# Kernel optimization log

Hardware: AMD Instinct MI355X
Metric: run time of the kernel (lower is better)

## Reference

```python
import jax, jax.numpy as jnp
from jax import lax
import numpy as np

EPS_START, EPS_END, EPS_DECAY = 1.0, 0.05, 10000.0


def gru_step(x, h, w_ih, w_hh, b_ih, b_hh):
    # PyTorch GRUCell math; gates stacked as [r, z, n]
    gi = x @ w_ih.T + b_ih
    gh = h @ w_hh.T + b_hh
    i_r, i_z, i_n = jnp.split(gi, 3, axis=1)
    h_r, h_z, h_n = jnp.split(gh, 3, axis=1)
    r = jax.nn.sigmoid(i_r + h_r)
    z = jax.nn.sigmoid(i_z + h_z)
    n = jnp.tanh(i_n + r * h_n)
    return (1.0 - z) * n + z * h


def setup_inputs() -> dict:
    key = jax.random.key(0)
    ks = jax.random.split(key, 7)
    V, E, H = 32000, 256, 512
    s = 0.05
    return {
        "embedding": jax.random.normal(ks[0], (V, E), jnp.float32) * s,
        "w_ih": jax.random.normal(ks[1], (3 * H, E), jnp.float32) * s,
        "w_hh": jax.random.normal(ks[2], (3 * H, H), jnp.float32) * s,
        "b_ih": jax.random.normal(ks[3], (3 * H,), jnp.float32) * s,
        "b_hh": jax.random.normal(ks[4], (3 * H,), jnp.float32) * s,
        "w_out": jax.random.normal(ks[5], (V, H), jnp.float32) * s,
        "b_out": jax.random.normal(ks[6], (V,), jnp.float32) * s,
        "seq_len": 256,
        "batch_size": 512,
    }


def reference(embedding, w_ih, w_hh, b_ih, b_hh, w_out, b_out, seq_len, batch_size):
    V, E = embedding.shape
    H = w_hh.shape[1]
    B = batch_size
    log_unif = jnp.float32(np.log(V))  # -log(vocab_size) fill for epsilon-greedy

    keys = jax.random.split(jax.random.key(42), seq_len)
    ts = jnp.arange(seq_len, dtype=jnp.float32)

    h0 = jnp.zeros((B, H), jnp.float32)
    x0 = jnp.broadcast_to(embedding[0], (B, E))  # start token id 0

    def step(carry, inp):
        h, x = carry
        t, k = inp
        k_eps, k_gum = jax.random.split(k)
        h = gru_step(x, h, w_ih, w_hh, b_ih, b_hh)
        logp = jax.nn.log_softmax(h @ w_out.T + b_out, axis=1)  # [B, V]
        eps_t = EPS_END + (EPS_START - EPS_END) * jnp.exp(-4.0 * t / EPS_DECAY)
        draw = eps_t >= jax.random.uniform(k_eps, (B,))
        masked = jnp.where(draw[:, None], -log_unif, logp)
        g = jax.random.gumbel(k_gum, (B, V), jnp.float32)
        sampled = jnp.argmax(masked + g, axis=1)  # [B] int
        lp = jnp.take_along_axis(logp, sampled[:, None], axis=1)[:, 0]
        x_next = embedding[sampled]
        return (h, x_next), (sampled, lp)

    _, (samples, lps) = lax.scan(step, (h0, x0), (ts, keys))
    return samples.T, lps.T  # [B, S] each
```

## Files before the change

kernel.cpp:

```cpp
#include <hip/hip_runtime.h>
#include <math.h>
#include <stdio.h>

#ifndef JAX_PARTITIONABLE
#define JAX_PARTITIONABLE 1
#endif

namespace {

constexpr int B  = 512;
constexpr int S  = 256;
constexpr int E  = 256;
constexpr int H  = 512;
constexpr int V  = 32000;
constexpr int G3 = 3 * H;
constexpr int VBLK = 64;
constexpr int BBLK = 256;
constexpr int NCH  = V / VBLK;
constexpr int NDMAX = 96;

typedef __bf16 bf16x8 __attribute__((ext_vector_type(8)));
typedef float  f32x4  __attribute__((ext_vector_type(4)));
typedef unsigned u32x4 __attribute__((ext_vector_type(4)));

__device__ __forceinline__ void tf2x32(unsigned k0, unsigned k1,
                                       unsigned x0, unsigned x1,
                                       unsigned& o0, unsigned& o1) {
  unsigned ks2 = k0 ^ k1 ^ 0x1BD11BDAu;
  x0 += k0; x1 += k1;
#define TFR(r) { x0 += x1; x1 = (x1 << (r)) | (x1 >> (32 - (r))); x1 ^= x0; }
  TFR(13) TFR(15) TFR(26) TFR(6)   x0 += k1;  x1 += ks2 + 1u;
  TFR(17) TFR(29) TFR(16) TFR(24)  x0 += ks2; x1 += k0 + 2u;
  TFR(13) TFR(15) TFR(26) TFR(6)   x0 += k0;  x1 += k1 + 3u;
  TFR(17) TFR(29) TFR(16) TFR(24)  x0 += k1;  x1 += ks2 + 4u;
  TFR(13) TFR(15) TFR(26) TFR(6)   x0 += ks2; x1 += k0 + 5u;
#undef TFR
  o0 = x0; o1 = x1;
}

__device__ __forceinline__ unsigned rbits(unsigned g0, unsigned g1,
                                          unsigned b, unsigned v) {
#if JAX_PARTITIONABLE
  unsigned y0, y1;
  tf2x32(g0, g1, 0u, b * (unsigned)V + v, y0, y1);
  return y0 ^ y1;
#else
  const unsigned N2 = (unsigned)(B/2) * (unsigned)V;
  unsigned ii = b * (unsigned)V + v;
  unsigned jj = (b < 256) ? ii : ii - N2;
  unsigned y0, y1;
  tf2x32(g0, g1, jj, N2 + jj, y0, y1);
  return (b < 256) ? y0 : y1;
#endif
}

__device__ __forceinline__ float u01_from_bits(unsigned bits) {
  return __uint_as_float(0x3f800000u | (bits >> 9)) - 1.0f;
}

__device__ __forceinline__ float gumbel_exact(unsigned bits) {
  float u = u01_from_bits(bits);
  if (u == 0.0f) u = 1.1754943508222875e-38f;
  float w = (float)(-log((double)u));
  return (float)(-log((double)w));
}

__device__ __forceinline__ float gumbel_fast(unsigned bits) {
  float u = u01_from_bits(bits);
  if (u == 0.0f) u = 1.1754943508222875e-38f;
  float w = -__logf(u);
  return -__logf(w);
}

__device__ __forceinline__ unsigned short f2bf(float f) {
  unsigned u = __float_as_uint(f);
  unsigned r = (u + 0x7fffu + ((u >> 16) & 1u)) >> 16;
  return (unsigned short)r;
}

__device__ __forceinline__ void glds16(const unsigned short* g,
                                       unsigned short* l) {
  __builtin_amdgcn_global_load_lds(
      (const __attribute__((address_space(1))) unsigned int*)g,
      (__attribute__((address_space(3))) unsigned int*)l, 16, 0, 0);
}

__device__ __forceinline__ size_t frag_off(int row, int k, int kTiles) {
  return ((size_t)((row >> 4) * kTiles + (k >> 5)) * 64
          + (row & 15) + 16 * ((k >> 3) & 3)) * 8 + (k & 7);
}

__global__ void k_init_rng(unsigned* __restrict__ kq, unsigned* __restrict__ ke) {
  int t = threadIdx.x;
  unsigned h0, h1, e0, e1, g0, g1;
#if JAX_PARTITIONABLE
  tf2x32(0u, 42u, 0u, (unsigned)t, h0, h1);
  tf2x32(h0, h1, 0u, 0u, e0, e1);
  tf2x32(h0, h1, 0u, 1u, g0, g1);
#else
  unsigned a0, a1, b0, b1;
  if (t < 128) {
    tf2x32(0u, 42u, (unsigned)(2*t),   (unsigned)(256+2*t), a0, a1);
    tf2x32(0u, 42u, (unsigned)(2*t+1), (unsigned)(257+2*t), b0, b1);
    h0 = a0; h1 = b0;
  } else {
    int j = 2*t - 256;
    tf2x32(0u, 42u, (unsigned)j,     (unsigned)(256+j), a0, a1);
    tf2x32(0u, 42u, (unsigned)(j+1), (unsigned)(257+j), b0, b1);
    h0 = a1; h1 = b1;
  }
  unsigned p0, p1, q0, q1;
  tf2x32(h0, h1, 0u, 2u, p0, p1);
  tf2x32(h0, h1, 1u, 3u, q0, q1);
  e0 = p0; e1 = q0; g0 = p1; g1 = q1;
#endif
  ke[2*t] = e0; ke[2*t+1] = e1;
  kq[2*t] = g0; kq[2*t+1] = g1;
}

__global__ void k_init_draws(const unsigned* __restrict__ ke,
                             unsigned char* __restrict__ draws) {
  int t = blockIdx.x;
  int b = threadIdx.x;
  unsigned k0 = ke[2*t], k1 = ke[2*t+1];
  unsigned bits, y0, y1;
#if JAX_PARTITIONABLE
  tf2x32(k0, k1, 0u, (unsigned)b, y0, y1);
  bits = y0 ^ y1;
#else
  if (b < 256) { tf2x32(k0, k1, (unsigned)b,       (unsigned)(256+b), y0, y1); bits = y0; }
  else         { tf2x32(k0, k1, (unsigned)(b-256), (unsigned)b,       y0, y1); bits = y1; }
#endif
  float u   = u01_from_bits(bits);
  float tf  = (float)t;
  float ex  = expf(__fmul_rn(-4.0f, tf) / 10000.0f);
  float eps = __fadd_rn(0.05f, __fmul_rn(0.95f, ex));
  draws[t*B + b] = (eps >= u) ? 1 : 0;
}

__global__ void k_init_nd(const unsigned char* __restrict__ draws,
                          int* __restrict__ nd_slot) {
  int t = blockIdx.x;
  if (threadIdx.x != 0) return;
  int cnt = 0;
  for (int b = 0; b < B; b++) {
    if (!draws[t*B + b] && cnt < NDMAX) nd_slot[t*B + b] = cnt++;
    else nd_slot[t*B + b] = -1;
  }
}

__global__ __launch_bounds__(256) void k_pre_argmax(
    const unsigned* __restrict__ kq, const unsigned char* __restrict__ draws,
    int* __restrict__ pre) {
  const int job  = blockIdx.x * 4 + (threadIdx.x >> 6);
  const int lane = threadIdx.x & 63;
  const int t = job >> 9, b = job & (B - 1);
  if (!draws[t*B + b]) { if (lane == 0) pre[job] = -1; return; }
  const unsigned g0 = kq[2*t], g1 = kq[2*t+1];
  unsigned best = 0u; int bv = V;
  for (int v = lane; v < V; v += 64) {
    unsigned bits = rbits(g0, g1, (unsigned)b, (unsigned)v) >> 9;
    if (bits > best || (bits == best && v < bv)) { best = bits; bv = v; }
  }
#pragma unroll
  for (int m = 1; m < 64; m <<= 1) {
    unsigned ob = __shfl_xor(best, m, 64);
    int      ov = __shfl_xor(bv,   m, 64);
    if (ob > best || (ob == best && ov < bv)) { best = ob; bv = ov; }
  }
  if (lane == 0) pre[job] = bv;
}

__global__ void k_init_state(const float* __restrict__ emb,
                             float* __restrict__ x, float* __restrict__ h) {
  int b = blockIdx.x, tid = threadIdx.x;
  x[b*E + tid] = emb[tid];
  h[b*H + tid] = 0.0f;
  h[b*H + 256 + tid] = 0.0f;
}

__global__ void k_cast_w(const float* __restrict__ w,
                         unsigned short* __restrict__ w_sw) {
  int g = blockIdx.x*256 + threadIdx.x;
  int v  = g >> 6;
  int k0 = (g & 63) * 8;
  const float* src = w + (size_t)v*H + k0;
  union { unsigned short s[8]; u32x4 vv; } u;
#pragma unroll
  for (int e = 0; e < 8; e++) u.s[e] = f2bf(src[e]);
  *(u32x4*)&w_sw[frag_off(v, k0, H/32)] = u.vv;
}

__global__ __launch_bounds__(256) void k_gates(
    const float* __restrict__ x, const float* __restrict__ h,
    const float* __restrict__ w_ih, const float* __restrict__ w_hh,
    const float* __restrict__ b_ih, const float* __restrict__ b_hh,
    float* __restrict__ gi, float* __restrict__ gh) {
  const int z = blockIdx.z;
  const float* A    = z ? h    : x;
  const float* W    = z ? w_hh : w_ih;
  const float* bias = z ? b_hh : b_ih;
  float*       C    = z ? gh   : gi;
  const int K       = z ? H    : E;

  __shared__ __align__(16) float As[16][68];
  __shared__ __align__(16) float Ws[16][68];
  const int tid = threadIdx.x;
  const int tx = tid & 15, ty = tid >> 4;
  const int row0 = blockIdx.y * 64, col0 = blockIdx.x * 64;
  float acc[4][4] = {};
  for (int k0 = 0; k0 < K; k0 += 16) {
#pragma unroll
    for (int l = 0; l < 4; l++) {
      int idx = tid + l*256;
      int r = idx >> 4, kk = idx & 15;
      As[kk][r] = A[(row0 + r)*K + k0 + kk];
      Ws[kk][r] = W[(col0 + r)*K + k0 + kk];
    }
    __syncthreads();
#pragma unroll
    for (int kk = 0; kk < 16; kk++) {
      const float4 av = *(const float4*)&As[kk][ty*4];
      const float4 wv = *(const float4*)&Ws[kk][tx*4];
      const float a[4] = {av.x, av.y, av.z, av.w};
      const float w[4] = {wv.x, wv.y, wv.z, wv.w};
#pragma unroll
      for (int i = 0; i < 4; i++)
#pragma unroll
        for (int j = 0; j < 4; j++) acc[i][j] = fmaf(a[i], w[j], acc[i][j]);
    }
    __syncthreads();
  }
#pragma unroll
  for (int i = 0; i < 4; i++) {
    int r = row0 + ty*4 + i;
#pragma unroll
    for (int j = 0; j < 4; j++) {
      int c = col0 + tx*4 + j;
      C[r*G3 + c] = __fadd_rn(acc[i][j], bias[c]);
    }
  }
}

__device__ __forceinline__ float sigm_acc(float v) {
  return (float)(1.0 / (1.0 + exp(-(double)v)));
}
__device__ __forceinline__ float tanh_acc(float v) {
  return (float)tanh((double)v);
}

__global__ void k_gru_update(const float* __restrict__ gi,
                             const float* __restrict__ gh,
                             float* __restrict__ h,
                             unsigned short* __restrict__ h_sw) {
  int g = blockIdx.x*256 + threadIdx.x;
  int b  = g >> 6;
  int j0 = (g & 63) * 8;
  const float* gib = gi + (size_t)b*G3;
  const float* ghb = gh + (size_t)b*G3;
  float hn[8];
  union { unsigned short s[8]; u32x4 vv; } u;
#pragma unroll
  for (int e = 0; e < 8; e++) {
    int j = j0 + e;
    float r  = sigm_acc(__fadd_rn(gib[j],     ghb[j]));
    float zz = sigm_acc(__fadd_rn(gib[H+j],   ghb[H+j]));
    float nn = tanh_acc(__fadd_rn(gib[2*H+j], __fmul_rn(r, ghb[2*H+j])));
    float hv = h[(size_t)b*H + j];
    float t1 = __fmul_rn(__fsub_rn(1.0f, zz), nn);
    float t2 = __fmul_rn(zz, hv);
    hn[e] = __fadd_rn(t1, t2);
    u.s[e] = f2bf(hn[e]);
  }
#pragma unroll
  for (int e = 0; e < 8; e++) h[(size_t)b*H + j0 + e] = hn[e];
  *(u32x4*)&h_sw[frag_off(b, j0, H/32)] = u.vv;
}

__global__ __launch_bounds__(256) void k_mfma_logits(
    const unsigned short* __restrict__ h_sw,
    const unsigned short* __restrict__ w_sw,
    const float* __restrict__ b_out,
    const unsigned* __restrict__ kq,
    const int* __restrict__ pre_t,
    const int* __restrict__ nd_slot_t,
    float* __restrict__ pmax, float* __restrict__ psum,
    float* __restrict__ plog,
    float* __restrict__ nd_keys, float* __restrict__ nd_kmax, int t) {
  const int vblk = blockIdx.x;
  const int bblk = blockIdx.y;
  const int tid  = threadIdx.x;
  const int lane = tid & 63, w = tid >> 6;
  const int quad = lane >> 4, l15 = lane & 15;

  __shared__ __align__(16) unsigned short wt[2][4*512];

  f32x4 acc[4][4] = {};

  const int mtBase = bblk*16 + w*4;
  const int ntBase = vblk*4;
  const unsigned short* hp = h_sw + (size_t)mtBase*16*512 + lane*8;
  const unsigned short* wstage = w_sw + (size_t)(ntBase + w)*16*512 + lane*8;
  unsigned short* ldst = &wt[0][0] + tid*8;

  glds16(wstage, ldst);
  bf16x8 afc[4];
#pragma unroll
  for (int mt = 0; mt < 4; mt++)
    afc[mt] = __builtin_bit_cast(bf16x8, *(const u32x4*)(hp + (size_t)(mt*16)*512));

#pragma unroll 1
  for (int kt = 0; kt < 15; kt++) {
    const int p = kt & 1;
    __syncthreads();
    glds16(wstage + (size_t)(kt + 1)*512, ldst + (p ^ 1)*2048);
    bf16x8 afn[4];
#pragma unroll
    for (int mt = 0; mt < 4; mt++)
      afn[mt] = __builtin_bit_cast(bf16x8,
          *(const u32x4*)(hp + (size_t)(mt*16 + kt + 1)*512));
    bf16x8 bfv[4];
#pragma unroll
    for (int nt = 0; nt < 4; nt++)
      bfv[nt] = __builtin_bit_cast(bf16x8,
          *(const u32x4*)&wt[p][nt*512 + lane*8]);
#pragma unroll
    for (int mt = 0; mt < 4; mt++)
#pragma unroll
      for (int nt = 0; nt < 4; nt++)
        acc[mt][nt] = __builtin_amdgcn_mfma_f32_16x16x32_bf16(
            afc[mt], bfv[nt], acc[mt][nt], 0, 0, 0);
#pragma unroll
    for (int mt = 0; mt < 4; mt++) afc[mt] = afn[mt];
  }
  {
    __syncthreads();
    bf16x8 bfv[4];
#pragma unroll
    for (int nt = 0; nt < 4; nt++)
      bfv[nt] = __builtin_bit_cast(bf16x8,
          *(const u32x4*)&wt[1][nt*512 + lane*8]);
#pragma unroll
    for (int mt = 0; mt < 4; mt++)
#pragma unroll
      for (int nt = 0; nt < 4; nt++)
        acc[mt][nt] = __builtin_amdgcn_mfma_f32_16x16x32_bf16(
            afc[mt], bfv[nt], acc[mt][nt], 0, 0, 0);
  }

  const int bW = bblk*256 + w*64;
  const int vW = vblk*64;
  const unsigned g0 = kq[2*t], g1 = kq[2*t+1];
  float bias[4];
#pragma unroll
  for (int nt = 0; nt < 4; nt++) bias[nt] = b_out[vW + nt*16 + l15];

#pragma unroll
  for (int mt = 0; mt < 4; mt++) {
#pragma unroll
    for (int r = 0; r < 4; r++) {
      const int b = bW + mt*16 + quad*4 + r;
      float lg[4];
#pragma unroll
      for (int nt = 0; nt < 4; nt++) lg[nt] = acc[mt][nt][r] + bias[nt];
      float lmax = fmaxf(fmaxf(lg[0], lg[1]), fmaxf(lg[2], lg[3]));
#pragma unroll
      for (int m = 1; m < 16; m <<= 1) lmax = fmaxf(lmax, __shfl_xor(lmax, m, 64));
      float ls = 0.0f;
#pragma unroll
      for (int nt = 0; nt < 4; nt++) ls += __expf(lg[nt] - lmax);
#pragma unroll
      for (int m = 1; m < 16; m <<= 1) ls += __shfl_xor(ls, m, 64);
      if (l15 == 0) { pmax[b*NCH + vblk] = lmax; psum[b*NCH + vblk] = ls; }
      const int pr = pre_t[b];
      if (pr >= 0) {
        int rel = pr - vW;
        if (rel >= 0 && rel < 64 && (rel & 15) == l15) plog[b] = lg[rel >> 4];
      } else {
        const int slot = nd_slot_t[b];
        if (slot >= 0) {
          float key[4];
#pragma unroll
          for (int nt = 0; nt < 4; nt++)
            key[nt] = lg[nt] + gumbel_fast(
                rbits(g0, g1, (unsigned)b, (unsigned)(vW + nt*16 + l15)));
          float* dst = nd_keys + (size_t)slot*V + vW + l15;
#pragma unroll
          for (int nt = 0; nt < 4; nt++) dst[nt*16] = key[nt];
          float kmx = fmaxf(fmaxf(key[0], key[1]), fmaxf(key[2], key[3]));
#pragma unroll
          for (int m = 1; m < 16; m <<= 1) kmx = fmaxf(kmx, __shfl_xor(kmx, m, 64));
          if (l15 == 0) nd_kmax[slot*NCH + vblk] = kmx;
        }
      }
    }
  }
}

__global__ __launch_bounds__(256) void k_finish(
    const float* __restrict__ pmax, const float* __restrict__ psum,
    const float* __restrict__ plog,
    const int* __restrict__ pre_t, const int* __restrict__ nd_slot_t,
    const float* __restrict__ nd_keys, const float* __restrict__ nd_kmax,
    const unsigned* __restrict__ kq,
    const float* __restrict__ h, const float* __restrict__ w_out,
    const float* __restrict__ b_out,
    const float* __restrict__ emb, float* __restrict__ x,
    float* __restrict__ out_samples, float* __restrict__ out_lps, int t) {
  const int b = blockIdx.x;
  const int tid = threadIdx.x;
  __shared__ float sA[256];
  __shared__ int   cand[160];
  __shared__ float cand_key[160], cand_lg[160];
  __shared__ int   ccnt;
  __shared__ int   s_samp;
  __shared__ float s_blog;

  float m = -INFINITY;
  for (int c = tid; c < NCH; c += 256) m = fmaxf(m, pmax[b*NCH + c]);
  sA[tid] = m; __syncthreads();
  for (int s = 128; s > 0; s >>= 1) {
    if (tid < s) sA[tid] = fmaxf(sA[tid], sA[tid+s]);
    __syncthreads();
  }
  const float M = sA[0];
  __syncthreads();
  float sum = 0.0f;
  for (int c = tid; c < NCH; c += 256)
    sum += psum[b*NCH + c] * expf(pmax[b*NCH + c] - M);
  sA[tid] = sum; __syncthreads();
  for (int s = 128; s > 0; s >>= 1) {
    if (tid < s) sA[tid] += sA[tid+s];
    __syncthreads();
  }
  const float SUM = sA[0];
  __syncthreads();

  const int pr = pre_t[b];
  if (pr >= 0) {
    if (tid == 0) { s_samp = pr; s_blog = plog[b]; }
  } else {
    const int slot = nd_slot_t[b];
    if (slot < 0) {
      if (tid == 0) { s_samp = 0; s_blog = plog[b]; }
    } else {
      const unsigned g0 = kq[2*t], g1 = kq[2*t+1];
      if (tid == 0) ccnt = 0;
      float km = -INFINITY;
      for (int c = tid; c < NCH; c += 256) km = fmaxf(km, nd_kmax[slot*NCH + c]);
      sA[tid] = km; __syncthreads();
      for (int s = 128; s > 0; s >>= 1) {
        if (tid < s) sA[tid] = fmaxf(sA[tid], sA[tid+s]);
        __syncthreads();
      }
      const float thr = sA[0] - 0.0859375f;
      __syncthreads();
      const float* keys = nd_keys + (size_t)slot*V;
      for (int c = tid; c < NCH; c += 256) {
        if (nd_kmax[slot*NCH + c] >= thr) {
          for (int j = 0; j < VBLK; j++) {
            float k = keys[c*VBLK + j];
            if (k >= thr) {
              int p = atomicAdd(&ccnt, 1);
              if (p < 160) cand[p] = c*VBLK + j;
            }
          }
        }
      }
      __syncthreads();
      const int nc = min(ccnt, 160);
      const int wid = tid >> 6, lane = tid & 63;
      for (int c = wid; c < nc; c += 4) {
        const int v = cand[c];
        const float* wr = w_out + (size_t)v*H;
        const float* hr = h + (size_t)b*H;
        float s = 0.0f;
#pragma unroll
        for (int i = 0; i < 8; i++) s = fmaf(hr[lane + 64*i], wr[lane + 64*i], s);
#pragma unroll
        for (int mm = 1; mm < 64; mm <<= 1) s += __shfl_xor(s, mm, 64);
        if (lane == 0) {
          float logit = __fadd_rn(s, b_out[v]);
          float key   = __fadd_rn(logit,
                          gumbel_exact(rbits(g0, g1, (unsigned)b, (unsigned)v)));
          cand_key[c] = key; cand_lg[c] = logit;
        }
      }
      __syncthreads();
      if (tid == 0) {
        float bk = -INFINITY; int bv = V; float bl = 0.0f;
        for (int c = 0; c < nc; c++) {
          float k = cand_key[c]; int v = cand[c];
          if (k > bk || (k == bk && v < bv)) { bk = k; bv = v; bl = cand_lg[c]; }
        }
        s_samp = bv; s_blog = bl;
      }
    }
  }
  __syncthreads();
  const int sampled = s_samp;
  if (tid == 0) {
    float lse = (float)log((double)SUM);
    float lp  = __fsub_rn(__fsub_rn(s_blog, M), lse);
    out_samples[b*S + t] = (float)sampled;
    out_lps[b*S + t]     = lp;
  }
  x[b*E + tid] = emb[sampled*E + tid];
}

}

extern "C" void kernel_launch(void* const* d_in, const int* in_sizes, int n_in,
                              void* d_out, int out_size, void* d_ws, size_t ws_size,
                              hipStream_t stream) {
  (void)in_sizes; (void)n_in; (void)out_size;
  const float* emb   = (const float*)d_in[0];
  const float* w_ih  = (const float*)d_in[1];
  const float* w_hh  = (const float*)d_in[2];
  const float* b_ih  = (const float*)d_in[3];
  const float* b_hh  = (const float*)d_in[4];
  const float* w_out = (const float*)d_in[5];
  const float* b_out = (const float*)d_in[6];
  float* out = (float*)d_out;

  char* wsb = (char*)d_ws;
  size_t off = 0;
  auto alloc = [&](size_t nbytes) {
    char* p = wsb + off;
    off += (nbytes + 255) & ~size_t(255);
    return p;
  };
  float* h     = (float*)alloc((size_t)B*H*4);
  float* x     = (float*)alloc((size_t)B*E*4);
  float* gi    = (float*)alloc((size_t)B*G3*4);
  float* gh    = (float*)alloc((size_t)B*G3*4);
  unsigned short* h_sw = (unsigned short*)alloc((size_t)B*H*2);
  unsigned short* w_sw = (unsigned short*)alloc((size_t)V*H*2);
  float* pmax  = (float*)alloc((size_t)B*NCH*4);
  float* psum  = (float*)alloc((size_t)B*NCH*4);
  float* plog  = (float*)alloc((size_t)B*4);
  unsigned* kq = (unsigned*)alloc((size_t)S*2*4);
  unsigned* ke = (unsigned*)alloc((size_t)S*2*4);
  unsigned char* draws = (unsigned char*)alloc((size_t)S*B);
  int* pre     = (int*)alloc((size_t)S*B*4);
  int* nd_slot = (int*)alloc((size_t)S*B*4);
  float* nd_keys = (float*)alloc((size_t)NDMAX*V*4);
  float* nd_kmax = (float*)alloc((size_t)NDMAX*NCH*4);
  if (off > ws_size) {
    fprintf(stderr, "kernel_launch: workspace too small (need %zu, have %zu)\n",
            off, ws_size);
    return;
  }

  k_init_rng<<<1, S, 0, stream>>>(kq, ke);
  k_init_draws<<<S, B, 0, stream>>>(ke, draws);
  k_init_nd<<<S, 64, 0, stream>>>(draws, nd_slot);
  k_pre_argmax<<<(S*B)/4, 256, 0, stream>>>(kq, draws, pre);
  k_init_state<<<B, 256, 0, stream>>>(emb, x, h);
  k_cast_w<<<(V*H/8)/256, 256, 0, stream>>>(w_out, w_sw);

  for (int t = 0; t < S; t++) {
    k_gates<<<dim3(G3/64, B/64, 2), 256, 0, stream>>>(x, h, w_ih, w_hh,
                                                      b_ih, b_hh, gi, gh);
    k_gru_update<<<(B*H/8)/256, 256, 0, stream>>>(gi, gh, h, h_sw);
    k_mfma_logits<<<dim3(V/VBLK, B/BBLK), 256, 0, stream>>>(
        h_sw, w_sw, b_out, kq, pre + t*B, nd_slot + t*B,
        pmax, psum, plog, nd_keys, nd_kmax, t);
    k_finish<<<B, 256, 0, stream>>>(pmax, psum, plog, pre + t*B, nd_slot + t*B,
                                    nd_keys, nd_kmax, kq, h, w_out, b_out,
                                    emb, x, out, out + (size_t)B*S, t);
  }
}
```

Baseline: 36.20 ms.

## Fuse next-step epsilon argmax into logits kernel, swizzle blocks, retile gates GEMM

The upfront k_pre_argmax over all timesteps is replaced. It now handles only step 0, and each later step's uniform-draw argmax runs in extra blocks of k_mfma_logits for timestep t+1, so that work overlaps the logits GEMM. The logits grid is remapped with an XCD-style swizzle of the linear block id into (vblk, bblk). k_gates moves to 512 threads computing 2x4 outputs each, with float4 stores. The risks are imbalance between the RNG blocks and the MFMA blocks, plus extra launched blocks that exit immediately.

```diff
diff --git a/kernel.cpp b/kernel.cpp
--- a/kernel.cpp
+++ b/kernel.cpp
@@ -191,7 +191,7 @@
   *(u32x4*)&w_sw[frag_off(v, k0, H/32)] = u.vv;
 }
 
-__global__ __launch_bounds__(256) void k_gates(
+__global__ __launch_bounds__(512) void k_gates(
     const float* __restrict__ x, const float* __restrict__ h,
     const float* __restrict__ w_ih, const float* __restrict__ w_hh,
     const float* __restrict__ b_ih, const float* __restrict__ b_hh,
@@ -208,11 +208,11 @@
   const int tid = threadIdx.x;
   const int tx = tid & 15, ty = tid >> 4;
   const int row0 = blockIdx.y * 64, col0 = blockIdx.x * 64;
-  float acc[4][4] = {};
+  float acc[2][4] = {};
   for (int k0 = 0; k0 < K; k0 += 16) {
 #pragma unroll
-    for (int l = 0; l < 4; l++) {
-      int idx = tid + l*256;
+    for (int l = 0; l < 2; l++) {
+      int idx = tid + l*512;
       int r = idx >> 4, kk = idx & 15;
       As[kk][r] = A[(row0 + r)*K + k0 + kk];
       Ws[kk][r] = W[(col0 + r)*K + k0 + kk];
@@ -220,25 +220,27 @@
     __syncthreads();
 #pragma unroll
     for (int kk = 0; kk < 16; kk++) {
-      const float4 av = *(const float4*)&As[kk][ty*4];
+      const float2 av = *(const float2*)&As[kk][ty*2];
       const float4 wv = *(const float4*)&Ws[kk][tx*4];
-      const float a[4] = {av.x, av.y, av.z, av.w};
+      const float a[2] = {av.x, av.y};
       const float w[4] = {wv.x, wv.y, wv.z, wv.w};
 #pragma unroll
-      for (int i = 0; i < 4; i++)
+      for (int i = 0; i < 2; i++)
 #pragma unroll
         for (int j = 0; j < 4; j++) acc[i][j] = fmaf(a[i], w[j], acc[i][j]);
     }
     __syncthreads();
   }
 #pragma unroll
-  for (int i = 0; i < 4; i++) {
-    int r = row0 + ty*4 + i;
-#pragma unroll
-    for (int j = 0; j < 4; j++) {
-      int c = col0 + tx*4 + j;
-      C[r*G3 + c] = __fadd_rn(acc[i][j], bias[c]);
-    }
+  for (int i = 0; i < 2; i++) {
+    int r = row0 + ty*2 + i;
+    int c = col0 + tx*4;
+    float4 o;
+    o.x = __fadd_rn(acc[i][0], bias[c + 0]);
+    o.y = __fadd_rn(acc[i][1], bias[c + 1]);
+    o.z = __fadd_rn(acc[i][2], bias[c + 2]);
+    o.w = __fadd_rn(acc[i][3], bias[c + 3]);
+    *(float4*)&C[r*G3 + c] = o;
   }
 }
 
@@ -282,18 +284,55 @@
     const unsigned short* __restrict__ w_sw,
     const float* __restrict__ b_out,
     const unsigned* __restrict__ kq,
-    const int* __restrict__ pre_t,
+    const unsigned char* __restrict__ draws,
+    int* __restrict__ pre,
     const int* __restrict__ nd_slot_t,
     float* __restrict__ pmax, float* __restrict__ psum,
     float* __restrict__ plog,
     float* __restrict__ nd_keys, float* __restrict__ nd_kmax, int t) {
-  const int vblk = blockIdx.x;
-  const int bblk = blockIdx.y;
+  __shared__ __align__(16) unsigned short wt[2][4*512];
   const int tid  = threadIdx.x;
+
+  if (blockIdx.y == 0) {
+    const int tn = t + 1;
+    if (tn >= S) return;
+    const int b = blockIdx.x;
+    if (!draws[tn*B + b]) { if (tid == 0) pre[tn*B + b] = -1; return; }
+    const unsigned g0 = kq[2*tn], g1 = kq[2*tn+1];
+    unsigned best = 0u; int bv = V;
+    for (int v = tid; v < V; v += 256) {
+      unsigned bits = rbits(g0, g1, (unsigned)b, (unsigned)v) >> 9;
+      if (bits > best || (bits == best && v < bv)) { best = bits; bv = v; }
+    }
+#pragma unroll
+    for (int m = 1; m < 64; m <<= 1) {
+      unsigned ob = __shfl_xor(best, m, 64);
+      int      ov = __shfl_xor(bv,   m, 64);
+      if (ob > best || (ob == best && ov < bv)) { best = ob; bv = ov; }
+    }
+    unsigned* sb = (unsigned*)&wt[0][0];
+    int*      sv = (int*)&wt[1][0];
+    const int wv2 = tid >> 6;
+    if ((tid & 63) == 0) { sb[wv2] = best; sv[wv2] = bv; }
+    __syncthreads();
+    if (tid == 0) {
+      for (int i = 1; i < 4; i++) {
+        unsigned ob = sb[i]; int ov = sv[i];
+        if (ob > best || (ob == best && ov < bv)) { best = ob; bv = ov; }
+      }
+      pre[tn*B + b] = bv;
+    }
+    return;
+  }
+
+  const int L  = (blockIdx.y - 1) * 512 + blockIdx.x;
+  const int wg = (L & 7) * 128 + (L >> 3);
+  if (wg >= 2*NCH) return;
+  const int vblk = wg >> 1;
+  const int bblk = wg & 1;
+  const int* __restrict__ pre_t = pre + t*B;
   const int lane = tid & 63, w = tid >> 6;
   const int quad = lane >> 4, l15 = lane & 15;
-
-  __shared__ __align__(16) unsigned short wt[2][4*512];
 
   f32x4 acc[4][4] = {};
 
@@ -555,16 +594,16 @@
   k_init_rng<<<1, S, 0, stream>>>(kq, ke);
   k_init_draws<<<S, B, 0, stream>>>(ke, draws);
   k_init_nd<<<S, 64, 0, stream>>>(draws, nd_slot);
-  k_pre_argmax<<<(S*B)/4, 256, 0, stream>>>(kq, draws, pre);
+  k_pre_argmax<<<B/4, 256, 0, stream>>>(kq, draws, pre);
   k_init_state<<<B, 256, 0, stream>>>(emb, x, h);
   k_cast_w<<<(V*H/8)/256, 256, 0, stream>>>(w_out, w_sw);
 
   for (int t = 0; t < S; t++) {
-    k_gates<<<dim3(G3/64, B/64, 2), 256, 0, stream>>>(x, h, w_ih, w_hh,
+    k_gates<<<dim3(G3/64, B/64, 2), 512, 0, stream>>>(x, h, w_ih, w_hh,
                                                       b_ih, b_hh, gi, gh);
     k_gru_update<<<(B*H/8)/256, 256, 0, stream>>>(gi, gh, h, h_sw);
-    k_mfma_logits<<<dim3(V/VBLK, B/BBLK), 256, 0, stream>>>(
-        h_sw, w_sw, b_out, kq, pre + t*B, nd_slot + t*B,
+    k_mfma_logits<<<dim3(512, 3), 256, 0, stream>>>(
+        h_sw, w_sw, b_out, kq, draws, pre, nd_slot + t*B,
         pmax, psum, plog, nd_keys, nd_kmax, t);
     k_finish<<<B, 256, 0, stream>>>(pmax, psum, plog, pre + t*B, nd_slot + t*B,
                                     nd_keys, nd_kmax, kq, h, w_out, b_out,
```

Measured after the change: 36.53 ms. No clear change (+0.9%).
